# Kernel optimization log

Measured on AMD Instinct MI355X. Metric: run time of the kernel, lower is better.

The kernel has to match this reference:

```python
import jax, jax.numpy as jnp
import numpy as np

N_FINE = 200000   # data.num_nodes (fine level)
N_COARSE = 50000  # nodes kept at coarse level
C = 128           # feature channels


def setup_inputs() -> dict:
    key = jax.random.key(0)
    x = jax.random.normal(key, (N_COARSE, 2, C, 2), dtype=jnp.float32)
    rng = np.random.default_rng(0)
    # coarse nodes are a subset of fine node ids
    unpool_nodes = np.sort(rng.permutation(N_FINE)[:N_COARSE]).astype(np.int32)
    # each fine node has exactly one unpool edge from some coarse node
    edge_src = unpool_nodes[rng.integers(0, N_COARSE, N_FINE)].astype(np.int32)
    edge_dst = rng.permutation(N_FINE).astype(np.int32)
    unpool_edges = jnp.asarray(np.stack([edge_src, edge_dst], axis=0))
    # unit complex parallel-transport rotations per edge
    theta = rng.uniform(0.0, 2.0 * np.pi, N_FINE).astype(np.float32)
    unpool_connection = jnp.asarray(np.stack([np.cos(theta), np.sin(theta)], axis=1))
    return {
        "x": x,
        "unpool_connection": unpool_connection,
        "unpool_nodes": jnp.asarray(unpool_nodes),
        "unpool_edges": unpool_edges,
        "num_nodes": N_FINE,
    }


def reference(x, unpool_connection, unpool_nodes, unpool_edges, num_nodes):
    n_coarse = unpool_nodes.shape[0]
    # unpool_map[fine_id_of_coarse_node] = coarse row index
    unpool_map = jnp.zeros((num_nodes,), dtype=jnp.int32).at[unpool_nodes].set(
        jnp.arange(n_coarse, dtype=jnp.int32))
    # gather coarse features per edge, scatter to fine node slots
    gathered = x[unpool_map[unpool_edges[0]]]               # [E, 2, C, 2]
    new_x = jnp.zeros((num_nodes,) + x.shape[1:], x.dtype).at[unpool_edges[1]].set(gathered)
    # align connection with fine node order (edges[1] is a permutation)
    connection = unpool_connection[jnp.argsort(unpool_edges[1])]  # [N, 2]
    # complex product on the order-1 stream: (a_re + i a_im) * (b_re - i b_im)
    a_re = new_x[:, 1, :, 0]            # [N, C]
    a_im = new_x[:, 1, :, 1]
    b_re = connection[:, None, 0]       # [N, 1]
    b_im = -connection[:, None, 1]
    out_re = a_re * b_re - a_im * b_im
    out_im = a_re * b_im + a_im * b_re
    new_x = new_x.at[:, 1, :, 0].set(out_re).at[:, 1, :, 1].set(out_im)
    return new_x
```

## Files before the change

### kernel.cpp

```cpp
#include <hip/hip_runtime.h>


typedef float v4f __attribute__((ext_vector_type(4)));

__global__ __launch_bounds__(256) void PTU_build_map_kernel(
    const int* __restrict__ nodes,
    int*       __restrict__ map,
    int n_coarse)
{
    int i = blockIdx.x * 256 + threadIdx.x;
    if (i < n_coarse) map[nodes[i]] = i;
}

__global__ __launch_bounds__(256) void PTU_build_rowinfo_kernel(
    const int*    __restrict__ map,
    const float2* __restrict__ conn,
    const int*    __restrict__ edge_src,
    const int*    __restrict__ edge_dst,
    float4*       __restrict__ rowinfo,
    int n_fine)
{
    int e = blockIdx.x * 256 + threadIdx.x;
    if (e >= n_fine) return;
    int s = edge_src[e];
    int d = edge_dst[e];
    int c = map[s];
    float2 b = conn[e];
    rowinfo[d] = make_float4(__int_as_float(c), b.x, b.y, 0.0f);
}

__global__ __launch_bounds__(256) void ParallelTransportUnpool_87582973100651_kernel(
    const float4* __restrict__ x,
    const float4* __restrict__ rowinfo,
    float4*       __restrict__ out,
    int n_fine)
{
    int wv = threadIdx.x >> 6;
    int r  = blockIdx.x * 4 + wv;
    if (r >= n_fine) return;
    int lane = threadIdx.x & 63;

    float4 info = rowinfo[r];
    int   c  = __builtin_amdgcn_readfirstlane(__float_as_int(info.x));
    float br = info.y;
    float bi = -info.z;

    const float4* __restrict__ xr = x + (size_t)c * 128;
    float4 v0 = xr[lane];
    float4 v1 = xr[lane + 64];

    float4 t;
    t.x = v1.x * br - v1.y * bi;
    t.y = v1.x * bi + v1.y * br;
    t.z = v1.z * br - v1.w * bi;
    t.w = v1.z * bi + v1.w * br;

    float4* orow = out + (size_t)r * 128;
    v4f nv0 = { v0.x, v0.y, v0.z, v0.w };
    v4f nv1 = { t.x,  t.y,  t.z,  t.w  };
    __builtin_nontemporal_store(nv0, reinterpret_cast<v4f*>(&orow[lane]));
    __builtin_nontemporal_store(nv1, reinterpret_cast<v4f*>(&orow[lane + 64]));
}

__global__ __launch_bounds__(256) void PTU_map_scatter_kernel(
    const float4* __restrict__ x,
    const float2* __restrict__ conn,
    const int*    __restrict__ map,
    const int*    __restrict__ edge_src,
    const int*    __restrict__ edge_dst,
    float4*       __restrict__ out,
    int n_fine)
{
    int wv = __builtin_amdgcn_readfirstlane(threadIdx.x >> 6);
    int e  = blockIdx.x * 4 + wv;
    if (e >= n_fine) return;
    int lane = threadIdx.x & 63;

    int s = __builtin_amdgcn_readfirstlane(edge_src[e]);
    int d = __builtin_amdgcn_readfirstlane(edge_dst[e]);
    int c = __builtin_amdgcn_readfirstlane(map[s]);

    const float4* __restrict__ xr = x + (size_t)c * 128;
    float4 v0 = xr[lane];
    float4 v1 = xr[lane + 64];
    float2 b  = conn[e];

    float br = b.x, bi = -b.y;
    float4 t;
    t.x = v1.x * br - v1.y * bi;
    t.y = v1.x * bi + v1.y * br;
    t.z = v1.z * br - v1.w * bi;
    t.w = v1.z * bi + v1.w * br;

    float4* orow = out + (size_t)d * 128;
    orow[lane]      = v0;
    orow[lane + 64] = t;
}

__global__ __launch_bounds__(256) void PTU_bsearch_kernel(
    const float4* __restrict__ x,
    const float2* __restrict__ conn,
    const int*    __restrict__ nodes,
    const int*    __restrict__ edge_src,
    const int*    __restrict__ edge_dst,
    float4*       __restrict__ out,
    int n_fine, int n_coarse)
{
    int e = blockIdx.x * 2 + (threadIdx.x >> 7);
    if (e >= n_fine) return;
    int lane = threadIdx.x & 127;

    int s = edge_src[e];
    int d = edge_dst[e];

    int lo = 0, hi = n_coarse - 1;
    while (lo < hi) {
        int mid = (lo + hi) >> 1;
        if (nodes[mid] < s) lo = mid + 1; else hi = mid;
    }
    int c = lo;

    float4 v = x[(size_t)c * 128 + lane];
    if (lane >= 64) {
        float2 b = conn[e];
        float br = b.x, bi = -b.y;
        float4 t;
        t.x = v.x * br - v.y * bi;
        t.y = v.x * bi + v.y * br;
        t.z = v.z * br - v.w * bi;
        t.w = v.z * bi + v.w * br;
        v = t;
    }
    out[(size_t)d * 128 + lane] = v;
}

extern "C" void kernel_launch(void* const* d_in, const int* in_sizes, int n_in,
                              void* d_out, int out_size, void* d_ws, size_t ws_size,
                              hipStream_t stream) {
    const float4* x     = (const float4*)d_in[0];
    const float2* conn  = (const float2*)d_in[1];
    const int*    nodes = (const int*)d_in[2];
    const int*    edges = (const int*)d_in[3];

    const int n_coarse = in_sizes[2];
    const int n_fine   = in_sizes[3] / 2;

    const int* edge_src = edges;
    const int* edge_dst = edges + n_fine;

    float4* out = (float4*)d_out;

    const size_t need_full = (size_t)n_fine * sizeof(float4) + (size_t)n_fine * sizeof(int);
    const size_t need_map  = (size_t)n_fine * sizeof(int);

    if (ws_size >= need_full) {
        float4* rowinfo = (float4*)d_ws;
        int*    map     = (int*)(rowinfo + n_fine);

        int mblocks = (n_coarse + 255) / 256;
        PTU_build_map_kernel<<<mblocks, 256, 0, stream>>>(nodes, map, n_coarse);

        int eblocks = (n_fine + 255) / 256;
        PTU_build_rowinfo_kernel<<<eblocks, 256, 0, stream>>>(
            map, conn, edge_src, edge_dst, rowinfo, n_fine);

        int blocks = (n_fine + 3) / 4;
        ParallelTransportUnpool_87582973100651_kernel<<<blocks, 256, 0, stream>>>(
            x, rowinfo, out, n_fine);
    } else if (ws_size >= need_map) {
        int* map = (int*)d_ws;
        int mblocks = (n_coarse + 255) / 256;
        PTU_build_map_kernel<<<mblocks, 256, 0, stream>>>(nodes, map, n_coarse);

        int blocks = (n_fine + 3) / 4;
        PTU_map_scatter_kernel<<<blocks, 256, 0, stream>>>(
            x, conn, map, edge_src, edge_dst, out, n_fine);
    } else {
        int blocks = (n_fine + 1) / 2;
        PTU_bsearch_kernel<<<blocks, 256, 0, stream>>>(
            x, conn, nodes, edge_src, edge_dst, out, n_fine, n_coarse);
    }
}
```

Before: 503.7 us.

## Bucket edges by coarse source to improve gather locality before unpool

Replaces the per-destination rowinfo table with a counting sort of edges into buckets of coarse source rows (count, scan, atomic scatter), so the main kernel reads x rows in roughly sorted order and scatters to destination rows instead. The aim is better cache and HBM locality on the 2 KB row gathers from x. In exchange it adds three kernel launches plus atomics, and the output writes become random instead of sequential.

Result: slower. 584.2 us (+16.0%).

```diff
diff --git a/kernel.cpp b/kernel.cpp
--- a/kernel.cpp
+++ b/kernel.cpp
@@ -2,6 +2,13 @@
 
 
 typedef float v4f __attribute__((ext_vector_type(4)));
+
+__global__ __launch_bounds__(256) void PTU_zero_kernel(
+    int* __restrict__ count, int nb)
+{
+    int i = blockIdx.x * 256 + threadIdx.x;
+    if (i < nb) count[i] = 0;
+}
 
 __global__ __launch_bounds__(256) void PTU_build_map_kernel(
     const int* __restrict__ nodes,
@@ -12,38 +19,70 @@
     if (i < n_coarse) map[nodes[i]] = i;
 }
 
-__global__ __launch_bounds__(256) void PTU_build_rowinfo_kernel(
+__global__ __launch_bounds__(256) void PTU_count_kernel(
+    const int* __restrict__ map,
+    const int* __restrict__ edge_src,
+    int*       __restrict__ count,
+    int n_fine, int shift)
+{
+    int e = blockIdx.x * 256 + threadIdx.x;
+    if (e >= n_fine) return;
+    int c = map[edge_src[e]];
+    atomicAdd(&count[c >> shift], 1);
+}
+
+__global__ __launch_bounds__(1024) void PTU_scan_kernel(
+    const int* __restrict__ count,
+    int*       __restrict__ tail,
+    int nb)
+{
+    __shared__ int sm[1024];
+    int t = threadIdx.x;
+    int v = (t < nb) ? count[t] : 0;
+    sm[t] = v;
+    __syncthreads();
+    for (int off = 1; off < 1024; off <<= 1) {
+        int add = (t >= off) ? sm[t - off] : 0;
+        __syncthreads();
+        sm[t] += add;
+        __syncthreads();
+    }
+    if (t < nb) tail[t] = sm[t] - v;
+}
+
+__global__ __launch_bounds__(256) void PTU_scatter_kernel(
     const int*    __restrict__ map,
     const float2* __restrict__ conn,
     const int*    __restrict__ edge_src,
     const int*    __restrict__ edge_dst,
-    float4*       __restrict__ rowinfo,
-    int n_fine)
+    int*          __restrict__ tail,
+    float4*       __restrict__ rec,
+    int n_fine, int shift)
 {
     int e = blockIdx.x * 256 + threadIdx.x;
     if (e >= n_fine) return;
-    int s = edge_src[e];
-    int d = edge_dst[e];
-    int c = map[s];
+    int c = map[edge_src[e]];
+    int pos = atomicAdd(&tail[c >> shift], 1);
     float2 b = conn[e];
-    rowinfo[d] = make_float4(__int_as_float(c), b.x, b.y, 0.0f);
+    rec[pos] = make_float4(__int_as_float(c), __int_as_float(edge_dst[e]), b.x, b.y);
 }
 
 __global__ __launch_bounds__(256) void ParallelTransportUnpool_87582973100651_kernel(
     const float4* __restrict__ x,
-    const float4* __restrict__ rowinfo,
+    const float4* __restrict__ rec,
     float4*       __restrict__ out,
     int n_fine)
 {
     int wv = threadIdx.x >> 6;
-    int r  = blockIdx.x * 4 + wv;
-    if (r >= n_fine) return;
+    int i  = blockIdx.x * 4 + wv;
+    if (i >= n_fine) return;
     int lane = threadIdx.x & 63;
 
-    float4 info = rowinfo[r];
-    int   c  = __builtin_amdgcn_readfirstlane(__float_as_int(info.x));
-    float br = info.y;
-    float bi = -info.z;
+    float4 rv = rec[i];
+    int   c  = __builtin_amdgcn_readfirstlane(__float_as_int(rv.x));
+    int   d  = __builtin_amdgcn_readfirstlane(__float_as_int(rv.y));
+    float br = rv.z;
+    float bi = -rv.w;
 
     const float4* __restrict__ xr = x + (size_t)c * 128;
     float4 v0 = xr[lane];
@@ -55,12 +94,13 @@
     t.z = v1.z * br - v1.w * bi;
     t.w = v1.z * bi + v1.w * br;
 
-    float4* orow = out + (size_t)r * 128;
+    float4* orow = out + (size_t)d * 128;
     v4f nv0 = { v0.x, v0.y, v0.z, v0.w };
     v4f nv1 = { t.x,  t.y,  t.z,  t.w  };
     __builtin_nontemporal_store(nv0, reinterpret_cast<v4f*>(&orow[lane]));
     __builtin_nontemporal_store(nv1, reinterpret_cast<v4f*>(&orow[lane + 64]));
 }
+
 
 __global__ __launch_bounds__(256) void PTU_map_scatter_kernel(
     const float4* __restrict__ x,
@@ -150,23 +190,35 @@
 
     float4* out = (float4*)d_out;
 
-    const size_t need_full = (size_t)n_fine * sizeof(float4) + (size_t)n_fine * sizeof(int);
-    const size_t need_map  = (size_t)n_fine * sizeof(int);
-
-    if (ws_size >= need_full) {
-        float4* rowinfo = (float4*)d_ws;
-        int*    map     = (int*)(rowinfo + n_fine);
+    int shift = 6;
+    while ((((long)n_coarse + (1 << shift) - 1) >> shift) > 1024) shift++;
+    const int nb = (n_coarse + (1 << shift) - 1) >> shift;
+
+    const size_t need_bucket = (size_t)n_fine * 16 + (size_t)n_fine * 4 + 2 * 1024 * 4;
+    const size_t need_map    = (size_t)n_fine * 4;
+
+    if (ws_size >= need_bucket) {
+        float4* rec   = (float4*)d_ws;
+        int*    map   = (int*)(rec + n_fine);
+        int*    count = map + n_fine;
+        int*    tail  = count + 1024;
+
+        PTU_zero_kernel<<<(nb + 255) / 256, 256, 0, stream>>>(count, nb);
 
         int mblocks = (n_coarse + 255) / 256;
         PTU_build_map_kernel<<<mblocks, 256, 0, stream>>>(nodes, map, n_coarse);
 
         int eblocks = (n_fine + 255) / 256;
-        PTU_build_rowinfo_kernel<<<eblocks, 256, 0, stream>>>(
-            map, conn, edge_src, edge_dst, rowinfo, n_fine);
+        PTU_count_kernel<<<eblocks, 256, 0, stream>>>(map, edge_src, count, n_fine, shift);
+
+        PTU_scan_kernel<<<1, 1024, 0, stream>>>(count, tail, nb);
+
+        PTU_scatter_kernel<<<eblocks, 256, 0, stream>>>(
+            map, conn, edge_src, edge_dst, tail, rec, n_fine, shift);
 
         int blocks = (n_fine + 3) / 4;
         ParallelTransportUnpool_87582973100651_kernel<<<blocks, 256, 0, stream>>>(
-            x, rowinfo, out, n_fine);
+            x, rec, out, n_fine);
     } else if (ws_size >= need_map) {
         int* map = (int*)d_ws;
         int mblocks = (n_coarse + 255) / 256;
```
